# Kernel tuning notes

Measured on AMD Instinct MI355X. Metric: run time of the kernel, lower is better.

The kernel has to match this reference:

```python
import jax, jax.numpy as jnp
import numpy as np

B, M, N = 16384, 512, 2048
N_ITERS = 10


def setup_inputs() -> dict:
    key = jax.random.key(0)
    kb, kD = jax.random.split(key)
    batch = jax.random.normal(kb, (B, M), dtype=jnp.float32)
    # nn.Parameter(torch.rand((M, N))) -> uniform [0,1)
    D = jax.random.uniform(kD, (M, N), dtype=jnp.float32)
    gamma = jnp.float32(0.1)
    beta = jnp.float32(0.1)
    return {"batch": batch, "D": D, "gamma": gamma, "beta": beta}


def reference(batch, D, gamma, beta):
    # Vectorized AMP sparse coding: the original loops over batch items; here
    # the per-sample matvecs D.T@v and D@alpha become batched GEMMs v@D, a@D.T.
    y = batch                                   # [B, M]
    m = D.shape[0]
    sqrt_m = jnp.sqrt(jnp.asarray(m, y.dtype))
    alpha0 = jnp.zeros((y.shape[0], D.shape[1]), dtype=y.dtype)  # [B, N]

    def amp_step(carry, _):
        alpha, v = carry
        z = alpha + beta * (v @ D)                               # [B, N]
        # per-sample threshold t = gamma/sqrt(M) * ||v||_2
        t = (gamma / sqrt_m) * jnp.linalg.norm(v, axis=-1, keepdims=True)  # [B,1]
        new_alpha = jnp.maximum(z - t, 0.0) * jnp.sign(z)        # relu(z-t)*sign(z)
        new_v = (y - beta * (new_alpha @ D.T)
                 + (beta / m) * jnp.linalg.norm(new_alpha, axis=-1, keepdims=True) * v)
        return (new_alpha, new_v), None

    (alpha, _v), _ = jax.lax.scan(amp_step, (alpha0, y), None, length=N_ITERS)
    return alpha
```

## Files before the change

kernel.cpp:

```cpp
#include <hip/hip_runtime.h>
#include <math.h>

#define Bsz 16384
#define Msz 512
#define Nsz 2048

typedef _Float16 half8 __attribute__((ext_vector_type(8)));
typedef _Float16 half4 __attribute__((ext_vector_type(4)));
typedef _Float16 half2v __attribute__((ext_vector_type(2)));
typedef float floatx16 __attribute__((ext_vector_type(16)));
typedef unsigned int uint;

struct HL { _Float16 h, l; };
__device__ __forceinline__ HL split1(float x) {
    HL r;
    r.h = (_Float16)x;
    r.l = (_Float16)(x - (float)r.h);
    return r;
}
__device__ __forceinline__ uint packHL(float x) {
    HL s = split1(x);
    return (uint)__builtin_bit_cast(unsigned short, s.h)
         | ((uint)__builtin_bit_cast(unsigned short, s.l) << 16);
}
__device__ __forceinline__ float unpackHL(uint w) {
    half2v p = __builtin_bit_cast(half2v, w);
    return (float)p.x + (float)p.y;
}

__device__ __forceinline__ void gl_lds16(const _Float16* g, _Float16* l) {
    __builtin_amdgcn_global_load_lds(
        (const __attribute__((address_space(1))) unsigned int*)g,
        (__attribute__((address_space(3))) unsigned int*)l, 16, 0, 0);
}

#define BAR()  asm volatile("s_barrier" ::: "memory")


__global__ __launch_bounds__(256) void zero_kernel(float4* __restrict__ p) {
    p[blockIdx.x * 256 + threadIdx.x] = make_float4(0.f, 0.f, 0.f, 0.f);
}

__global__ __launch_bounds__(256) void init_kernel(const float* __restrict__ batch,
        _Float16* __restrict__ vh, float* __restrict__ t2) {
    const int wave = threadIdx.x >> 6;
    const int lane = threadIdx.x & 63;
    const int b = (blockIdx.x << 2) + wave;
    const float* row = batch + (size_t)b * Msz + lane * 8;
    float4 a = *(const float4*)row;
    float4 c = *(const float4*)(row + 4);
    half8 h;
    h[0] = (_Float16)a.x; h[1] = (_Float16)a.y;
    h[2] = (_Float16)a.z; h[3] = (_Float16)a.w;
    h[4] = (_Float16)c.x; h[5] = (_Float16)c.y;
    h[6] = (_Float16)c.z; h[7] = (_Float16)c.w;
    const size_t off = ((size_t)(b >> 5) * 32 + (lane >> 1)) * 512
                     + ((size_t)(lane & 1) << 8) + ((b & 31) << 3);
    *(half8*)(vh + off) = h;
    float s = a.x*a.x + a.y*a.y + a.z*a.z + a.w*a.w
            + c.x*c.x + c.y*c.y + c.z*c.z + c.w*c.w;
#pragma unroll
    for (int off2 = 32; off2 > 0; off2 >>= 1) s += __shfl_down(s, off2);
    if (lane == 0) t2[b] = s;
}

__global__ __launch_bounds__(256) void convD_kernel(const float* __restrict__ D,
        _Float16* __restrict__ Dph, _Float16* __restrict__ Dtph) {
    __shared__ float T[64][65];
    const int t = threadIdx.x;
    const int tx = t & 15, ty = t >> 4;
    const int n0 = blockIdx.x << 6, m0 = blockIdx.y << 6;
#pragma unroll
    for (int q = 0; q < 4; ++q) {
        const int mr = m0 + (ty << 2) + q;
        const int nc = n0 + (tx << 2);
        float4 d = *(const float4*)(D + (size_t)mr * Nsz + nc);
        half4 h;
        h[0] = (_Float16)d.x; h[1] = (_Float16)d.y;
        h[2] = (_Float16)d.z; h[3] = (_Float16)d.w;
        const size_t o2 = ((size_t)(mr >> 5) * 128 + (nc >> 4)) * 512
                        + (((size_t)(nc >> 3) & 1) << 8) + ((mr & 31) << 3) + (nc & 7);
        *(half4*)(Dph + o2) = h;
        T[(tx << 2) + 0][(ty << 2) + q] = d.x;
        T[(tx << 2) + 1][(ty << 2) + q] = d.y;
        T[(tx << 2) + 2][(ty << 2) + q] = d.z;
        T[(tx << 2) + 3][(ty << 2) + q] = d.w;
    }
    __syncthreads();
#pragma unroll
    for (int q = 0; q < 4; ++q) {
        const int nr = n0 + (ty << 2) + q;
        const int mc = m0 + (tx << 2);
        float4 d = make_float4(T[(ty << 2) + q][tx << 2],
                               T[(ty << 2) + q][(tx << 2) + 1],
                               T[(ty << 2) + q][(tx << 2) + 2],
                               T[(ty << 2) + q][(tx << 2) + 3]);
        half4 h;
        h[0] = (_Float16)d.x; h[1] = (_Float16)d.y;
        h[2] = (_Float16)d.z; h[3] = (_Float16)d.w;
        const size_t o1 = ((size_t)(nr >> 5) * 32 + (mc >> 4)) * 512
                        + (((size_t)(mc >> 3) & 1) << 8) + ((nr & 31) << 3) + (mc & 7);
        *(half4*)(Dtph + o1) = h;
    }
}

template<int FIRST, int LAST>
__global__ __launch_bounds__(256, 4) void gemm1_kernel(
        const _Float16* __restrict__ Av,
        const _Float16* __restrict__ Bth,
        const float* __restrict__ t2,
        uint* __restrict__ alphaP,
        float* __restrict__ na2,
        const float* __restrict__ beta_p, const float* __restrict__ gamma_p) {
    __shared__ _Float16 lds[8192];

    const int tid = threadIdx.x;
    const int wave = tid >> 6, lane = tid & 63;
    const int wy = wave >> 1, wx = wave & 1;
    const int ln = lane & 31, lh = lane >> 5;
    const int bid = blockIdx.x;
    const int b0 = (bid & 127) << 7;
    const int n0 = (bid >> 7) << 7;
    const int R0 = b0 >> 5, C0 = n0 >> 5;

    floatx16 acc[2][2] = {};

    const _Float16* pb[4];
#pragma unroll
    for (int e = 0; e < 4; ++e) {
        const int f = wave * 4 + e;
        const bool isB = f >= 8;
        const int q = isB ? f - 8 : f;
        const int t = q >> 1, kt = q & 1;
        const _Float16* base = isB ? Bth : Av;
        const int T0 = isB ? C0 : R0;
        pb[e] = base + ((size_t)(T0 + t) * 32) * 512 + (size_t)kt * 512 + lane * 8;
    }
    const int f0 = wave * 4;

    const int ro = lane << 3;

    for (int c = 0; c < 16; ++c) {
        __syncthreads();
#pragma unroll
        for (int e = 0; e < 4; ++e)
            gl_lds16(pb[e] + (size_t)c * 1024, lds + ((f0 + e) << 9));
        __builtin_amdgcn_s_waitcnt(0);
        __syncthreads();

#pragma unroll
        for (int ks = 0; ks < 2; ++ks) {
            half8 fa[2], fb[2];
#pragma unroll
            for (int i = 0; i < 2; ++i) {
                fa[i] = *(const half8*)(lds + ((((wy * 2 + i) << 1) + ks) << 9) + ro);
                fb[i] = *(const half8*)(lds + 4096 + ((((wx * 2 + i) << 1) + ks) << 9) + ro);
            }
#pragma unroll
            for (int j = 0; j < 2; ++j)
#pragma unroll
                for (int i = 0; i < 2; ++i)
                    acc[i][j] = __builtin_amdgcn_mfma_f32_32x32x16_f16(fa[i], fb[j], acc[i][j], 0, 0, 0);
        }
    }

    const float beta = beta_p[0];
    const float tc = gamma_p[0] * 0.044194173824159216f;
#pragma unroll
    for (int i = 0; i < 2; ++i) {
#pragma unroll
        for (int reg = 0; reg < 16; ++reg) {
            const int rr = (reg & 3) + 8 * (reg >> 2) + 4 * lh;
            const int b = b0 + wy * 64 + i * 32 + rr;
            const float tb2 = tc * sqrtf(t2[b]);
            uint* arow = alphaP + (size_t)b * Nsz + n0 + wx * 64 + ln;
            float s = 0.f;
#pragma unroll
            for (int j = 0; j < 2; ++j) {
                float z = FIRST ? 0.f : unpackHL(arow[j * 32]);
                float val = fmaxf(fmaf(beta, acc[i][j][reg], z) - tb2, 0.f);
                if (LAST) ((float*)arow)[j * 32] = val;
                else      arow[j * 32] = packHL(val);
                s = fmaf(val, val, s);
            }
            s += __shfl_down(s, 16, 32);
            s += __shfl_down(s, 8, 32);
            s += __shfl_down(s, 4, 32);
            s += __shfl_down(s, 2, 32);
            s += __shfl_down(s, 1, 32);
            if (ln == 0) atomicAdd(&na2[b], s);
        }
    }
}

__global__ __launch_bounds__(256, 2) void gemm2_kernel(
        const uint* __restrict__ alphaP,
        const _Float16* __restrict__ Bh,
        const float* __restrict__ na2,
        const float* __restrict__ y,
        _Float16* __restrict__ vh,
        float* __restrict__ t2,
        const float* __restrict__ beta_p) {
    __shared__ _Float16 lds[16384];

    const int tid = threadIdx.x;
    const int wave = tid >> 6, lane = tid & 63;
    const int wy = wave >> 1, wx = wave & 1;
    const int ln = lane & 31, lh = lane >> 5;
    const int bid = blockIdx.x;
    const int b0 = (bid & 127) << 7;
    const int m0 = (bid >> 7) << 7;
    const int C0 = m0 >> 5;

    floatx16 acc[2][2] = {};

    const int srow = tid >> 1;
    const int skq  = (tid & 1) << 4;
    const uint* apP = alphaP + (size_t)(b0 + srow) * Nsz + skq;
    const int awo = ((((srow >> 5) << 1) + (skq >> 4)) << 9) + ((srow & 31) << 3);

    const _Float16* gB = Bh + ((size_t)(C0 + wave) * 128) * 512 + lane * 8;
    const int fB = 8 + wave * 2;

    const int ro = lane << 3;

    uint4 a0, a1, a2, a3;
    auto loadA = [&](int c) {
        const uint* nx = apP + c * 32;
        a0 = *(const uint4*)(nx);
        a1 = *(const uint4*)(nx + 4);
        a2 = *(const uint4*)(nx + 8);
        a3 = *(const uint4*)(nx + 12);
    };
    auto writeA = [&](int d) {
        uint4 ha, hb;
        ha.x = __builtin_amdgcn_perm(a0.y, a0.x, 0x05040100u);
        ha.y = __builtin_amdgcn_perm(a0.w, a0.z, 0x05040100u);
        ha.z = __builtin_amdgcn_perm(a1.y, a1.x, 0x05040100u);
        ha.w = __builtin_amdgcn_perm(a1.w, a1.z, 0x05040100u);
        hb.x = __builtin_amdgcn_perm(a2.y, a2.x, 0x05040100u);
        hb.y = __builtin_amdgcn_perm(a2.w, a2.z, 0x05040100u);
        hb.z = __builtin_amdgcn_perm(a3.y, a3.x, 0x05040100u);
        hb.w = __builtin_amdgcn_perm(a3.w, a3.z, 0x05040100u);
        _Float16* aw = lds + d * 8192 + awo;
        *(uint4*)aw = ha;
        *(uint4*)(aw + 256) = hb;
    };
    auto stageB = [&](int c, int d) {
        _Float16* lB = lds + d * 8192;
#pragma unroll
        for (int kt = 0; kt < 2; ++kt)
            gl_lds16(gB + (size_t)kt * 512 + (size_t)c * 1024, lB + ((fB + kt) << 9));
    };

    loadA(0);
    writeA(0);
    stageB(0, 0);
    loadA(1);
    writeA(1);
    stageB(1, 1);
    loadA(2);
    asm volatile("s_waitcnt vmcnt(6) lgkmcnt(0)" ::: "memory");
    BAR();

    for (int c = 0; c < 64; ++c) {
        const _Float16* lb = lds + (c & 1) * 8192;
        __builtin_amdgcn_s_setprio(1);
#pragma unroll
        for (int ks = 0; ks < 2; ++ks) {
            half8 fa[2], fb[2];
#pragma unroll
            for (int i = 0; i < 2; ++i) {
                fa[i] = *(const half8*)(lb + ((((wy * 2 + i) << 1) + ks) << 9) + ro);
                fb[i] = *(const half8*)(lb + 4096 + ((((wx * 2 + i) << 1) + ks) << 9) + ro);
            }
#pragma unroll
            for (int j = 0; j < 2; ++j)
#pragma unroll
                for (int i = 0; i < 2; ++i)
                    acc[i][j] = __builtin_amdgcn_mfma_f32_32x32x16_f16(fa[i], fb[j], acc[i][j], 0, 0, 0);
        }
        __builtin_amdgcn_s_setprio(0);
        if (c == 63) break;
        BAR();
        if (c < 61) {
            stageB(c + 2, c & 1);
            writeA(c & 1);
            loadA(c + 3);
            asm volatile("s_waitcnt vmcnt(6) lgkmcnt(0)" ::: "memory");
        } else if (c == 61) {
            stageB(63, 1);
            writeA(1);
            asm volatile("s_waitcnt vmcnt(2) lgkmcnt(0)" ::: "memory");
        } else {
            asm volatile("s_waitcnt vmcnt(0) lgkmcnt(0)" ::: "memory");
        }
        BAR();
    }

    const float beta = beta_p[0];
#pragma unroll
    for (int i = 0; i < 2; ++i) {
#pragma unroll
        for (int reg = 0; reg < 16; ++reg) {
            const int rr = (reg & 3) + 8 * (reg >> 2) + 4 * lh;
            const int b = b0 + wy * 64 + i * 32 + rr;
            const float cb = beta * (1.0f / 512.0f) * sqrtf(na2[b]);
            float s = 0.f;
#pragma unroll
            for (int j = 0; j < 2; ++j) {
                const int m = m0 + wx * 64 + j * 32 + ln;
                const size_t po = ((size_t)(b >> 5) * 32 + (m >> 4)) * 512
                                + (((size_t)(m >> 3) & 1) << 8) + ((b & 31) << 3) + (m & 7);
                const size_t yi = (size_t)b * Msz + m;
                float vold = (float)vh[po];
                float val = y[yi] - beta * acc[i][j][reg] + cb * vold;
                vh[po] = (_Float16)val;
                s = fmaf(val, val, s);
            }
            s += __shfl_down(s, 16, 32);
            s += __shfl_down(s, 8, 32);
            s += __shfl_down(s, 4, 32);
            s += __shfl_down(s, 2, 32);
            s += __shfl_down(s, 1, 32);
            if (ln == 0) atomicAdd(&t2[b], s);
        }
    }
}

extern "C" void kernel_launch(void* const* d_in, const int* in_sizes, int n_in,
                              void* d_out, int out_size, void* d_ws, size_t ws_size,
                              hipStream_t stream) {
    (void)in_sizes; (void)n_in; (void)out_size; (void)ws_size;
    const float* batch   = (const float*)d_in[0];
    const float* D       = (const float*)d_in[1];
    const float* gamma_p = (const float*)d_in[2];
    const float* beta_p  = (const float*)d_in[3];

    uint* alphaP = (uint*)d_out;

    _Float16* vh   = (_Float16*)d_ws;
    _Float16* Dph  = vh + (size_t)Bsz * Msz;
    _Float16* Dtph = Dph + (size_t)Msz * Nsz;
    float*    t2s  = (float*)(Dtph + (size_t)Msz * Nsz);
    float*    na2s = t2s + 10 * Bsz;

    zero_kernel<<<19 * Bsz / 1024, 256, 0, stream>>>((float4*)(t2s + Bsz));
    convD_kernel<<<dim3(Nsz / 64, Msz / 64), 256, 0, stream>>>(D, Dph, Dtph);
    init_kernel<<<Bsz / 4, 256, 0, stream>>>(batch, vh, t2s);

    for (int it = 0; it < 10; ++it) {
        if (it == 0)
            gemm1_kernel<1, 0><<<2048, 256, 0, stream>>>(vh, Dtph,
                    t2s + (size_t)it * Bsz, alphaP, na2s + (size_t)it * Bsz,
                    beta_p, gamma_p);
        else if (it == 9)
            gemm1_kernel<0, 1><<<2048, 256, 0, stream>>>(vh, Dtph,
                    t2s + (size_t)it * Bsz, alphaP, na2s + (size_t)it * Bsz,
                    beta_p, gamma_p);
        else
            gemm1_kernel<0, 0><<<2048, 256, 0, stream>>>(vh, Dtph,
                    t2s + (size_t)it * Bsz, alphaP, na2s + (size_t)it * Bsz,
                    beta_p, gamma_p);
        if (it < 9) {
            gemm2_kernel<<<512, 256, 0, stream>>>(alphaP, Dph,
                                                  na2s + (size_t)it * Bsz,
                                                  batch, vh,
                                                  t2s + (size_t)(it + 1) * Bsz,
                                                  beta_p);
        }
    }
}
```

Measured before the change: 1.626 ms.

## Load GEMM1 MFMA fragments directly from global with register double-buffering

Removes the shared-memory staging and block-wide barriers from the first GEMM kernel. Each wave now loads its own pre-swizzled A and B fragments straight from global memory into registers, double-buffered so the next k-step's loads are issued while the current MFMAs run. This drops LDS traffic and sync stalls, but each fragment is now read from global/L2 by two waves instead of once per block, which raises cache traffic.

After: 1.650 ms (median of 2 runs). About the same (+1.5%).

```diff
diff --git a/kernel.cpp b/kernel.cpp
--- a/kernel.cpp
+++ b/kernel.cpp
@@ -112,8 +112,6 @@
         uint* __restrict__ alphaP,
         float* __restrict__ na2,
         const float* __restrict__ beta_p, const float* __restrict__ gamma_p) {
-    __shared__ _Float16 lds[8192];
-
     const int tid = threadIdx.x;
     const int wave = tid >> 6, lane = tid & 63;
     const int wy = wave >> 1, wx = wave & 1;
@@ -125,42 +123,43 @@
 
     floatx16 acc[2][2] = {};
 
-    const _Float16* pb[4];
-#pragma unroll
-    for (int e = 0; e < 4; ++e) {
-        const int f = wave * 4 + e;
-        const bool isB = f >= 8;
-        const int q = isB ? f - 8 : f;
-        const int t = q >> 1, kt = q & 1;
-        const _Float16* base = isB ? Bth : Av;
-        const int T0 = isB ? C0 : R0;
-        pb[e] = base + ((size_t)(T0 + t) * 32) * 512 + (size_t)kt * 512 + lane * 8;
-    }
-    const int f0 = wave * 4;
-
-    const int ro = lane << 3;
-
-    for (int c = 0; c < 16; ++c) {
-        __syncthreads();
-#pragma unroll
-        for (int e = 0; e < 4; ++e)
-            gl_lds16(pb[e] + (size_t)c * 1024, lds + ((f0 + e) << 9));
-        __builtin_amdgcn_s_waitcnt(0);
-        __syncthreads();
-
-#pragma unroll
-        for (int ks = 0; ks < 2; ++ks) {
-            half8 fa[2], fb[2];
-#pragma unroll
-            for (int i = 0; i < 2; ++i) {
-                fa[i] = *(const half8*)(lds + ((((wy * 2 + i) << 1) + ks) << 9) + ro);
-                fb[i] = *(const half8*)(lds + 4096 + ((((wx * 2 + i) << 1) + ks) << 9) + ro);
+    const _Float16* pa0 = Av  + ((size_t)(R0 + 2 * wy)     * 32) * 512 + lane * 8;
+    const _Float16* pa1 = Av  + ((size_t)(R0 + 2 * wy + 1) * 32) * 512 + lane * 8;
+    const _Float16* pb0 = Bth + ((size_t)(C0 + 2 * wx)     * 32) * 512 + lane * 8;
+    const _Float16* pb1 = Bth + ((size_t)(C0 + 2 * wx + 1) * 32) * 512 + lane * 8;
+
+    half8 xa0, xa1, xb0, xb1;
+    half8 ya0, ya1, yb0, yb1;
+
+    xa0 = *(const half8*)(pa0);
+    xa1 = *(const half8*)(pa1);
+    xb0 = *(const half8*)(pb0);
+    xb1 = *(const half8*)(pb1);
+
+    for (int kt = 0; kt < 32; kt += 2) {
+        {
+            const size_t o = (size_t)(kt + 1) << 9;
+            ya0 = *(const half8*)(pa0 + o);
+            ya1 = *(const half8*)(pa1 + o);
+            yb0 = *(const half8*)(pb0 + o);
+            yb1 = *(const half8*)(pb1 + o);
+            acc[0][0] = __builtin_amdgcn_mfma_f32_32x32x16_f16(xa0, xb0, acc[0][0], 0, 0, 0);
+            acc[1][0] = __builtin_amdgcn_mfma_f32_32x32x16_f16(xa1, xb0, acc[1][0], 0, 0, 0);
+            acc[0][1] = __builtin_amdgcn_mfma_f32_32x32x16_f16(xa0, xb1, acc[0][1], 0, 0, 0);
+            acc[1][1] = __builtin_amdgcn_mfma_f32_32x32x16_f16(xa1, xb1, acc[1][1], 0, 0, 0);
+        }
+        {
+            if (kt + 2 < 32) {
+                const size_t o = (size_t)(kt + 2) << 9;
+                xa0 = *(const half8*)(pa0 + o);
+                xa1 = *(const half8*)(pa1 + o);
+                xb0 = *(const half8*)(pb0 + o);
+                xb1 = *(const half8*)(pb1 + o);
             }
-#pragma unroll
-            for (int j = 0; j < 2; ++j)
-#pragma unroll
-                for (int i = 0; i < 2; ++i)
-                    acc[i][j] = __builtin_amdgcn_mfma_f32_32x32x16_f16(fa[i], fb[j], acc[i][j], 0, 0, 0);
+            acc[0][0] = __builtin_amdgcn_mfma_f32_32x32x16_f16(ya0, yb0, acc[0][0], 0, 0, 0);
+            acc[1][0] = __builtin_amdgcn_mfma_f32_32x32x16_f16(ya1, yb0, acc[1][0], 0, 0, 0);
+            acc[0][1] = __builtin_amdgcn_mfma_f32_32x32x16_f16(ya0, yb1, acc[0][1], 0, 0, 0);
+            acc[1][1] = __builtin_amdgcn_mfma_f32_32x32x16_f16(ya1, yb1, acc[1][1], 0, 0, 0);
         }
     }
 
```
